# Performance work log

Hardware: AMD Instinct MI355X
Metric: run time of the kernel (lower is better)

The kernel has to match this reference:

```python
import jax, jax.numpy as jnp
import numpy as np

DECAY_FACTOR = 0.995  # temporal decay applied to similarities
MIN_SIMILARITY = 0.0

BATCH, FEAT_DIM = 256, 128
CAPACITY, HORIZON, NUM_FEATURES = 100000, 24, 7


def _l2_normalize(x, eps=1e-12):
    # matches torch F.normalize(p=2): divide by max(||x||, eps)
    n = jnp.linalg.norm(x, axis=-1, keepdims=True)
    return x / jnp.maximum(n, eps)


def setup_inputs() -> dict:
    key = jax.random.key(0)
    k1, k2, k3, k4 = jax.random.split(key, 4)
    return {
        "query": jax.random.normal(k1, (BATCH, FEAT_DIM), dtype=jnp.float32),
        "keys": jax.random.normal(k2, (CAPACITY, FEAT_DIM), dtype=jnp.float32),
        "values": jax.random.normal(k3, (CAPACITY, HORIZON, NUM_FEATURES), dtype=jnp.float32),
        "timestamps": jax.random.randint(k4, (CAPACITY,), 0, 1000, dtype=jnp.int32),
        "global_step": 1000,
        "top_k": 5,
    }


def reference(query, keys, values, timestamps, global_step, top_k):
    """ErrorMemoryBank.retrieve with a full bank (n == capacity),
    no trajectory bias, min_similarity=0."""
    q_norm = _l2_normalize(query)            # [B, D]
    k_norm = _l2_normalize(keys)             # [C, D]
    sims = jnp.einsum('bd,cd->bc', q_norm, k_norm)  # [B, C] cosine sims

    age = (jnp.asarray(global_step, jnp.int32) - timestamps).astype(jnp.float32)  # [C]
    decay = jnp.power(jnp.float32(DECAY_FACTOR), age)                              # [C]
    sims = sims * decay[None, :]

    top_sims, top_idx = jax.lax.top_k(sims, top_k)   # [B, K], [B, K]
    retrieved = values[top_idx]                      # gather -> [B, K, H, F]
    valid_mask = top_sims >= MIN_SIMILARITY          # [B, K]
    return retrieved, top_sims, valid_mask, top_idx
```

## Files before the change

### kernel.cpp

```cpp
#include <hip/hip_runtime.h>
#include <math.h>

#define BATCH 256
#define FEAT 128
#define CAP 100000
#define ROWF 168
#define K 5
#define NBLKG 1564
#define NCHK 6256
#define NCHKR 6250
#define SCPT 7
#define MAXSEL 48
#define MARGIN 0.008f

#define OUT_SIMS 215040
#define OUT_MASK 216320
#define OUT_IDX  217600

#define WS_QF    0
#define WS_TMAX  16384

typedef __attribute__((ext_vector_type(8))) short short8;
typedef __attribute__((ext_vector_type(4))) float f32x4;

#define BET(vs,vi,ss,ii) ((vs) > (ss) || ((vs) == (ss) && (vi) < (ii)))

__device__ __forceinline__ unsigned pack2(float a, float b) {
  unsigned ua = (__float_as_uint(a) + 0x8000u) >> 16;
  unsigned ub = (__float_as_uint(b) + 0x8000u) & 0xffff0000u;
  return ua | ub;
}

__device__ __forceinline__ void ins_val(float v, float (&s)[5]) {
  if (v > s[4]) {
    float x = v;
    #pragma unroll
    for (int j = 0; j < 5; ++j) {
      float hi = fmaxf(s[j], x);
      x = fminf(s[j], x);
      s[j] = hi;
    }
  }
}

__device__ __forceinline__ void ins_cmp(float v, int k, float (&s)[5], int (&i)[5]) {
  if (BET(v,k,s[4],i[4])) {
    if (BET(v,k,s[3],i[3])) { s[4]=s[3]; i[4]=i[3];
      if (BET(v,k,s[2],i[2])) { s[3]=s[2]; i[3]=i[2];
        if (BET(v,k,s[1],i[1])) { s[2]=s[1]; i[2]=i[1];
          if (BET(v,k,s[0],i[0])) { s[1]=s[0]; i[1]=i[0]; s[0]=v; i[0]=k; }
          else { s[1]=v; i[1]=k; } }
        else { s[2]=v; i[2]=k; } }
      else { s[3]=v; i[3]=k; } }
    else { s[4]=v; i[4]=k; }
  }
}

__global__ __launch_bounds__(256) void prep_q(const float* __restrict__ query,
                                              uint4* __restrict__ qF) {
  int b = blockIdx.x, tid = threadIdx.x;
  int rid = tid >> 4, dp = tid & 15;
  int q_ = b*16 + rid;
  const float4* src = reinterpret_cast<const float4*>(query + (size_t)q_*FEAT + dp*8);
  float4 v0 = src[0], v1 = src[1];
  float ss = v0.x*v0.x + v0.y*v0.y + v0.z*v0.z + v0.w*v0.w
           + v1.x*v1.x + v1.y*v1.y + v1.z*v1.z + v1.w*v1.w;
  ss += __shfl_xor(ss,1); ss += __shfl_xor(ss,2);
  ss += __shfl_xor(ss,4); ss += __shfl_xor(ss,8);
  float inv = 1.0f / fmaxf(sqrtf(ss), 1e-12f);
  v0.x*=inv; v0.y*=inv; v0.z*=inv; v0.w*=inv;
  v1.x*=inv; v1.y*=inv; v1.z*=inv; v1.w*=inv;
  uint4 pk;
  pk.x = pack2(v0.x,v0.y); pk.y = pack2(v0.z,v0.w);
  pk.z = pack2(v1.x,v1.y); pk.w = pack2(v1.z,v1.w);
  int s_ = dp >> 2, lg = dp & 3;
  qF[(b*4 + s_)*64 + lg*16 + rid] = pk;
}

__global__ __launch_bounds__(512, 4) void gemm_max6(
    const float* __restrict__ keys, const int* __restrict__ ts,
    const int* __restrict__ gstep, const uint4* __restrict__ qF,
    float* __restrict__ tmax) {
  __shared__ uint4 lds_kf[16*66];
  __shared__ float sscale[64];
  int tid = threadIdx.x;
  int w = tid >> 6, lane = tid & 63;
  int blk = blockIdx.x;
  int kbase = blk * 64;
  int g0 = gstep[0];

  short8 qf0[4], qf1[4];
  #pragma unroll
  for (int s_ = 0; s_ < 4; ++s_) {
    qf0[s_] = __builtin_bit_cast(short8, qF[((2*w  )*4 + s_)*64 + lane]);
    qf1[s_] = __builtin_bit_cast(short8, qF[((2*w+1)*4 + s_)*64 + lane]);
  }

  int dp = tid & 15;
  #pragma unroll
  for (int it = 0; it < 2; ++it) {
    int kl = it*32 + (tid >> 4);
    int gk = kbase + kl;
    int gkc = gk < CAP ? gk : CAP-1;
    const float4* kp = reinterpret_cast<const float4*>(keys + (size_t)gkc*FEAT + dp*8);
    float4 v0 = kp[0], v1 = kp[1];
    float ss = v0.x*v0.x+v0.y*v0.y+v0.z*v0.z+v0.w*v0.w
             + v1.x*v1.x+v1.y*v1.y+v1.z*v1.z+v1.w*v1.w;
    ss += __shfl_xor(ss,1); ss += __shfl_xor(ss,2);
    ss += __shfl_xor(ss,4); ss += __shfl_xor(ss,8);
    if (dp == 0) {
      float scl = 0.0f;
      if (gk < CAP) {
        float age = (float)(g0 - ts[gk]);
        scl = exp2f(age * -0.00723157f) * __frsqrt_rn(fmaxf(ss, 1e-24f));
      }
      sscale[kl] = scl;
    }
    uint4 pk;
    pk.x = pack2(v0.x, v0.y); pk.y = pack2(v0.z, v0.w);
    pk.z = pack2(v1.x, v1.y); pk.w = pack2(v1.z, v1.w);
    int slab = (kl >> 4)*4 + (dp >> 2);
    int slot = (dp & 3)*16 + (kl & 15);
    lds_kf[slab*66 + slot] = pk;
  }
  __syncthreads();

  float tm0[4], tm1[4];
  #pragma unroll
  for (int t = 0; t < 4; ++t) {
    f32x4 acc0 = {0.f,0.f,0.f,0.f}, acc1 = {0.f,0.f,0.f,0.f};
    #pragma unroll
    for (int s_ = 0; s_ < 4; ++s_) {
      short8 a = __builtin_bit_cast(short8, lds_kf[(t*4 + s_)*66 + lane]);
      acc0 = __builtin_amdgcn_mfma_f32_16x16x32_bf16(a, qf0[s_], acc0, 0,0,0);
      acc1 = __builtin_amdgcn_mfma_f32_16x16x32_bf16(a, qf1[s_], acc1, 0,0,0);
    }
    int kbl = t*16 + (lane>>4)*4;
    float4 sc = *reinterpret_cast<float4*>(&sscale[kbl]);
    float m0 = fmaxf(fmaxf(acc0[0]*sc.x, acc0[1]*sc.y),
                     fmaxf(acc0[2]*sc.z, acc0[3]*sc.w));
    float m1 = fmaxf(fmaxf(acc1[0]*sc.x, acc1[1]*sc.y),
                     fmaxf(acc1[2]*sc.z, acc1[3]*sc.w));
    m0 = fmaxf(m0, __shfl_xor(m0,16)); m0 = fmaxf(m0, __shfl_xor(m0,32));
    m1 = fmaxf(m1, __shfl_xor(m1,16)); m1 = fmaxf(m1, __shfl_xor(m1,32));
    tm0[t] = m0; tm1[t] = m1;
  }

  if (lane < 16) {
    int q0 = w*32 + lane, q1 = q0 + 16;
    float4 a0 = {tm0[0],tm0[1],tm0[2],tm0[3]};
    float4 b0 = {tm1[0],tm1[1],tm1[2],tm1[3]};
    *reinterpret_cast<float4*>(&tmax[(size_t)q0*NCHK + blk*4]) = a0;
    *reinterpret_cast<float4*>(&tmax[(size_t)q1*NCHK + blk*4]) = b0;
  }
}

__global__ __launch_bounds__(1024) void select_rescore4(
    const float* __restrict__ tmax, const float* __restrict__ keys,
    const float* __restrict__ query, const int* __restrict__ ts,
    const int* __restrict__ gstep, const float* __restrict__ values,
    float* __restrict__ out) {
  int q = blockIdx.x, tid = threadIdx.x;
  int w = tid >> 6, lane = tid & 63;
  int gstep0 = gstep[0];

  __shared__ float qrow[FEAT];
  if (tid < 16) {
    int d0 = tid * 8;
    const float4* src = reinterpret_cast<const float4*>(query + (size_t)q*FEAT + d0);
    float4 v0 = src[0], v1 = src[1];
    float ss = v0.x*v0.x + v0.y*v0.y + v0.z*v0.z + v0.w*v0.w
             + v1.x*v1.x + v1.y*v1.y + v1.z*v1.z + v1.w*v1.w;
    ss += __shfl_xor(ss,1); ss += __shfl_xor(ss,2);
    ss += __shfl_xor(ss,4); ss += __shfl_xor(ss,8);
    float inv = 1.0f / fmaxf(sqrtf(ss), 1e-12f);
    v0.x*=inv; v0.y*=inv; v0.z*=inv; v0.w*=inv;
    v1.x*=inv; v1.y*=inv; v1.z*=inv; v1.w*=inv;
    float4* dst = reinterpret_cast<float4*>(qrow + d0);
    dst[0] = v0; dst[1] = v1;
  }
  __syncthreads();

  float cs[SCPT];
  #pragma unroll
  for (int j = 0; j < SCPT; ++j) {
    int c = tid + j*1024;
    cs[j] = (c < NCHKR) ? tmax[(size_t)q*NCHK + c] : -INFINITY;
  }
  float s5[5] = {-INFINITY,-INFINITY,-INFINITY,-INFINITY,-INFINITY};
  #pragma unroll
  for (int j = 0; j < SCPT; ++j) ins_val(cs[j], s5);
  #pragma unroll
  for (int off = 1; off < 64; off <<= 1) {
    float ps[5];
    #pragma unroll
    for (int j=0;j<5;++j) ps[j] = __shfl_xor(s5[j], off);
    #pragma unroll
    for (int j=0;j<5;++j) ins_val(ps[j], s5);
  }
  __shared__ float rS[16][5]; __shared__ int rI[16][5];
  if (lane == 0) {
    #pragma unroll
    for (int j=0;j<5;++j) rS[w][j] = s5[j];
  }
  __syncthreads();
  __shared__ float thSh;
  if (w == 0) {
    float m5[5] = {-INFINITY,-INFINITY,-INFINITY,-INFINITY,-INFINITY};
    if (lane < 16) {
      #pragma unroll
      for (int j=0;j<5;++j) m5[j] = rS[lane][j];
    }
    #pragma unroll
    for (int off = 1; off < 16; off <<= 1) {
      float ps[5];
      #pragma unroll
      for (int j=0;j<5;++j) ps[j] = __shfl_xor(m5[j], off);
      #pragma unroll
      for (int j=0;j<5;++j) ins_val(ps[j], m5);
    }
    if (lane == 0) thSh = m5[4] - MARGIN;
  }
  __syncthreads();
  float th = thSh;

  __shared__ int cnt; __shared__ int clist[MAXSEL];
  if (tid == 0) cnt = 0;
  __syncthreads();
  #pragma unroll
  for (int j = 0; j < SCPT; ++j) {
    int c = tid + j*1024;
    if (c < NCHKR && cs[j] >= th) {
      int p = atomicAdd(&cnt, 1);
      if (p < MAXSEL) clist[p] = c;
    }
  }
  __syncthreads();
  int nsel = cnt < MAXSEL ? cnt : MAXSEL;

  __shared__ float exs[MAXSEL*16];
  for (int s4 = tid; s4 < nsel*64; s4 += 1024) {
    int slot = s4 >> 2, part = s4 & 3;
    int key = clist[slot >> 4]*16 + (slot & 15);
    float dot = 0.f, ksq = 0.f;
    if (key < CAP) {
      const float4* kp = reinterpret_cast<const float4*>(keys + (size_t)key*FEAT + part*32);
      const float4* qp = reinterpret_cast<float4*>(qrow) + part*8;
      #pragma unroll
      for (int d = 0; d < 8; ++d) {
        float4 kv = kp[d];
        float4 qv = qp[d];
        dot = fmaf(kv.w,qv.w,fmaf(kv.z,qv.z,fmaf(kv.y,qv.y,fmaf(kv.x,qv.x,dot))));
        ksq = fmaf(kv.w,kv.w,fmaf(kv.z,kv.z,fmaf(kv.y,kv.y,fmaf(kv.x,kv.x,ksq))));
      }
    }
    dot += __shfl_xor(dot,1); dot += __shfl_xor(dot,2);
    ksq += __shfl_xor(ksq,1); ksq += __shfl_xor(ksq,2);
    if (part == 0) {
      float sim = -INFINITY;
      if (key < CAP) {
        float age = (float)(gstep0 - ts[key]);
        sim = dot / fmaxf(sqrtf(ksq), 1e-12f) * powf(0.995f, age);
      }
      exs[slot] = sim;
    }
  }
  __syncthreads();

  float fs5[5] = {-INFINITY,-INFINITY,-INFINITY,-INFINITY,-INFINITY};
  int   fi5[5] = {0x7fffffff,0x7fffffff,0x7fffffff,0x7fffffff,0x7fffffff};
  if (tid < nsel*16) {
    fs5[0] = exs[tid];
    fi5[0] = clist[tid >> 4]*16 + (tid & 15);
  }
  #pragma unroll
  for (int off = 1; off < 64; off <<= 1) {
    float ps[5]; int pi[5];
    #pragma unroll
    for (int j=0;j<5;++j){ ps[j]=__shfl_xor(fs5[j],off); pi[j]=__shfl_xor(fi5[j],off); }
    #pragma unroll
    for (int j=0;j<5;++j) ins_cmp(ps[j], pi[j], fs5, fi5);
  }
  if (lane == 0) {
    #pragma unroll
    for (int j=0;j<5;++j){ rS[w][j]=fs5[j]; rI[w][j]=fi5[j]; }
  }
  __syncthreads();
  __shared__ int wix[K];
  if (w == 0) {
    float fs[5] = {-INFINITY,-INFINITY,-INFINITY,-INFINITY,-INFINITY};
    int   fi[5] = {0x7fffffff,0x7fffffff,0x7fffffff,0x7fffffff,0x7fffffff};
    if (lane < 16) {
      #pragma unroll
      for (int j=0;j<5;++j){ fs[j]=rS[lane][j]; fi[j]=rI[lane][j]; }
    }
    #pragma unroll
    for (int off = 1; off < 16; off <<= 1) {
      float ps[5]; int pi[5];
      #pragma unroll
      for (int j=0;j<5;++j){ ps[j]=__shfl_xor(fs[j],off); pi[j]=__shfl_xor(fi[j],off); }
      #pragma unroll
      for (int j=0;j<5;++j) ins_cmp(ps[j], pi[j], fs, fi);
    }
    if (lane == 0) {
      #pragma unroll
      for (int r = 0; r < K; ++r) {
        out[OUT_SIMS + q*K + r] = fs[r];
        out[OUT_MASK + q*K + r] = (fs[r] >= 0.0f) ? 1.0f : 0.0f;
        out[OUT_IDX  + q*K + r] = (float)fi[r];
        wix[r] = fi[r];
      }
    }
  }
  __syncthreads();
  for (int idx = tid; idx < K*ROWF; idx += 1024) {
    int r = idx / ROWF, e = idx - r*ROWF;
    out[(q*K + r)*ROWF + e] = values[(size_t)wix[r]*ROWF + e];
  }
}

extern "C" void kernel_launch(void* const* d_in, const int* in_sizes, int n_in,
                              void* d_out, int out_size, void* d_ws, size_t ws_size,
                              hipStream_t stream) {
  const float* query  = (const float*)d_in[0];
  const float* keys   = (const float*)d_in[1];
  const float* values = (const float*)d_in[2];
  const int*   ts     = (const int*)d_in[3];
  const int*   gstep  = (const int*)d_in[4];

  float* out  = (float*)d_out;
  float* wsf  = (float*)d_ws;
  uint4* qF   = (uint4*)(wsf + WS_QF);
  float* tmax = wsf + WS_TMAX;

  prep_q<<<16, 256, 0, stream>>>(query, qF);
  gemm_max6<<<NBLKG, 512, 0, stream>>>(keys, ts, gstep, qF, tmax);
  select_rescore4<<<BATCH, 1024, 0, stream>>>(tmax, keys, query, ts, gstep, values, out);
}
```

Before: 46.54 us.

## Fuse three kernels into one persistent kernel with a grid barrier

```diff
diff --git a/kernel.cpp b/kernel.cpp
--- a/kernel.cpp
+++ b/kernel.cpp
@@ -6,7 +6,8 @@
 #define CAP 100000
 #define ROWF 168
 #define K 5
-#define NBLKG 1564
+#define NBLOCKS 256
+#define NCHKB 1564
 #define NCHK 6256
 #define NCHKR 6250
 #define SCPT 7
@@ -17,8 +18,8 @@
 #define OUT_MASK 216320
 #define OUT_IDX  217600
 
-#define WS_QF    0
-#define WS_TMAX  16384
+#define WS_TMAX 0
+#define WS_BAR  1601536
 
 typedef __attribute__((ext_vector_type(8))) short short8;
 typedef __attribute__((ext_vector_type(4))) float f32x4;
@@ -56,115 +57,125 @@
   }
 }
 
-__global__ __launch_bounds__(256) void prep_q(const float* __restrict__ query,
-                                              uint4* __restrict__ qF) {
-  int b = blockIdx.x, tid = threadIdx.x;
-  int rid = tid >> 4, dp = tid & 15;
-  int q_ = b*16 + rid;
-  const float4* src = reinterpret_cast<const float4*>(query + (size_t)q_*FEAT + dp*8);
-  float4 v0 = src[0], v1 = src[1];
-  float ss = v0.x*v0.x + v0.y*v0.y + v0.z*v0.z + v0.w*v0.w
-           + v1.x*v1.x + v1.y*v1.y + v1.z*v1.z + v1.w*v1.w;
-  ss += __shfl_xor(ss,1); ss += __shfl_xor(ss,2);
-  ss += __shfl_xor(ss,4); ss += __shfl_xor(ss,8);
-  float inv = 1.0f / fmaxf(sqrtf(ss), 1e-12f);
-  v0.x*=inv; v0.y*=inv; v0.z*=inv; v0.w*=inv;
-  v1.x*=inv; v1.y*=inv; v1.z*=inv; v1.w*=inv;
-  uint4 pk;
-  pk.x = pack2(v0.x,v0.y); pk.y = pack2(v0.z,v0.w);
-  pk.z = pack2(v1.x,v1.y); pk.w = pack2(v1.z,v1.w);
-  int s_ = dp >> 2, lg = dp & 3;
-  qF[(b*4 + s_)*64 + lg*16 + rid] = pk;
-}
-
-__global__ __launch_bounds__(512, 4) void gemm_max6(
-    const float* __restrict__ keys, const int* __restrict__ ts,
-    const int* __restrict__ gstep, const uint4* __restrict__ qF,
-    float* __restrict__ tmax) {
-  __shared__ uint4 lds_kf[16*66];
-  __shared__ float sscale[64];
+__global__ __launch_bounds__(1024, 4) void fused_all(
+    const float* __restrict__ query, const float* __restrict__ keys,
+    const float* __restrict__ values, const int* __restrict__ ts,
+    const int* __restrict__ gstep, float* __restrict__ tmax,
+    unsigned* __restrict__ bar, float* __restrict__ out) {
+  __shared__ uint4 shmem[4096];
+  __shared__ __attribute__((aligned(16))) float sscale[2][64];
+  __shared__ float qrow[FEAT];
+  __shared__ float rS[16][5]; __shared__ int rI[16][5];
+  __shared__ float thSh;
+  __shared__ int cnt_s; __shared__ int clist[MAXSEL];
+  __shared__ float exs[MAXSEL*16];
+  __shared__ int wix[K];
+
   int tid = threadIdx.x;
   int w = tid >> 6, lane = tid & 63;
   int blk = blockIdx.x;
-  int kbase = blk * 64;
   int g0 = gstep[0];
 
-  short8 qf0[4], qf1[4];
-  #pragma unroll
-  for (int s_ = 0; s_ < 4; ++s_) {
-    qf0[s_] = __builtin_bit_cast(short8, qF[((2*w  )*4 + s_)*64 + lane]);
-    qf1[s_] = __builtin_bit_cast(short8, qF[((2*w+1)*4 + s_)*64 + lane]);
-  }
-
+  {
+    int dp = lane & 15;
+    #pragma unroll
+    for (int it = 0; it < 4; ++it) {
+      int rid = it*4 + (lane >> 4);
+      int q_ = w*16 + rid;
+      const float4* src = reinterpret_cast<const float4*>(query + (size_t)q_*FEAT + dp*8);
+      float4 v0 = src[0], v1 = src[1];
+      float ss = v0.x*v0.x + v0.y*v0.y + v0.z*v0.z + v0.w*v0.w
+               + v1.x*v1.x + v1.y*v1.y + v1.z*v1.z + v1.w*v1.w;
+      ss += __shfl_xor(ss,1); ss += __shfl_xor(ss,2);
+      ss += __shfl_xor(ss,4); ss += __shfl_xor(ss,8);
+      float inv = 1.0f / fmaxf(sqrtf(ss), 1e-12f);
+      v0.x*=inv; v0.y*=inv; v0.z*=inv; v0.w*=inv;
+      v1.x*=inv; v1.y*=inv; v1.z*=inv; v1.w*=inv;
+      uint4 pk;
+      pk.x = pack2(v0.x,v0.y); pk.y = pack2(v0.z,v0.w);
+      pk.z = pack2(v1.x,v1.y); pk.w = pack2(v1.z,v1.w);
+      shmem[w*256 + (dp>>2)*64 + (dp&3)*16 + rid] = pk;
+    }
+  }
+  __syncthreads();
+  short8 qf[4];
+  #pragma unroll
+  for (int s_ = 0; s_ < 4; ++s_)
+    qf[s_] = __builtin_bit_cast(short8, shmem[w*256 + s_*64 + lane]);
+  __syncthreads();
+
+  int kl = tid >> 4;
   int dp = tid & 15;
-  #pragma unroll
-  for (int it = 0; it < 2; ++it) {
-    int kl = it*32 + (tid >> 4);
-    int gk = kbase + kl;
+  float4 kv0, kv1; int tsv = 0;
+  auto ld = [&](int cb) {
+    int gk = cb*64 + kl;
     int gkc = gk < CAP ? gk : CAP-1;
     const float4* kp = reinterpret_cast<const float4*>(keys + (size_t)gkc*FEAT + dp*8);
-    float4 v0 = kp[0], v1 = kp[1];
-    float ss = v0.x*v0.x+v0.y*v0.y+v0.z*v0.z+v0.w*v0.w
-             + v1.x*v1.x+v1.y*v1.y+v1.z*v1.z+v1.w*v1.w;
+    kv0 = kp[0]; kv1 = kp[1];
+    if (dp == 0 && gk < CAP) tsv = ts[gk];
+  };
+  int buf = 0;
+  int cb = blk;
+  ld(cb);
+  while (cb < NCHKB) {
+    float ss = kv0.x*kv0.x+kv0.y*kv0.y+kv0.z*kv0.z+kv0.w*kv0.w
+             + kv1.x*kv1.x+kv1.y*kv1.y+kv1.z*kv1.z+kv1.w*kv1.w;
     ss += __shfl_xor(ss,1); ss += __shfl_xor(ss,2);
     ss += __shfl_xor(ss,4); ss += __shfl_xor(ss,8);
     if (dp == 0) {
       float scl = 0.0f;
+      int gk = cb*64 + kl;
       if (gk < CAP) {
-        float age = (float)(g0 - ts[gk]);
+        float age = (float)(g0 - tsv);
         scl = exp2f(age * -0.00723157f) * __frsqrt_rn(fmaxf(ss, 1e-24f));
       }
-      sscale[kl] = scl;
+      sscale[buf][kl] = scl;
     }
     uint4 pk;
-    pk.x = pack2(v0.x, v0.y); pk.y = pack2(v0.z, v0.w);
-    pk.z = pack2(v1.x, v1.y); pk.w = pack2(v1.z, v1.w);
+    pk.x = pack2(kv0.x, kv0.y); pk.y = pack2(kv0.z, kv0.w);
+    pk.z = pack2(kv1.x, kv1.y); pk.w = pack2(kv1.z, kv1.w);
     int slab = (kl >> 4)*4 + (dp >> 2);
     int slot = (dp & 3)*16 + (kl & 15);
-    lds_kf[slab*66 + slot] = pk;
-  }
-  __syncthreads();
-
-  float tm0[4], tm1[4];
-  #pragma unroll
-  for (int t = 0; t < 4; ++t) {
-    f32x4 acc0 = {0.f,0.f,0.f,0.f}, acc1 = {0.f,0.f,0.f,0.f};
-    #pragma unroll
-    for (int s_ = 0; s_ < 4; ++s_) {
-      short8 a = __builtin_bit_cast(short8, lds_kf[(t*4 + s_)*66 + lane]);
-      acc0 = __builtin_amdgcn_mfma_f32_16x16x32_bf16(a, qf0[s_], acc0, 0,0,0);
-      acc1 = __builtin_amdgcn_mfma_f32_16x16x32_bf16(a, qf1[s_], acc1, 0,0,0);
-    }
-    int kbl = t*16 + (lane>>4)*4;
-    float4 sc = *reinterpret_cast<float4*>(&sscale[kbl]);
-    float m0 = fmaxf(fmaxf(acc0[0]*sc.x, acc0[1]*sc.y),
-                     fmaxf(acc0[2]*sc.z, acc0[3]*sc.w));
-    float m1 = fmaxf(fmaxf(acc1[0]*sc.x, acc1[1]*sc.y),
-                     fmaxf(acc1[2]*sc.z, acc1[3]*sc.w));
-    m0 = fmaxf(m0, __shfl_xor(m0,16)); m0 = fmaxf(m0, __shfl_xor(m0,32));
-    m1 = fmaxf(m1, __shfl_xor(m1,16)); m1 = fmaxf(m1, __shfl_xor(m1,32));
-    tm0[t] = m0; tm1[t] = m1;
-  }
-
-  if (lane < 16) {
-    int q0 = w*32 + lane, q1 = q0 + 16;
-    float4 a0 = {tm0[0],tm0[1],tm0[2],tm0[3]};
-    float4 b0 = {tm1[0],tm1[1],tm1[2],tm1[3]};
-    *reinterpret_cast<float4*>(&tmax[(size_t)q0*NCHK + blk*4]) = a0;
-    *reinterpret_cast<float4*>(&tmax[(size_t)q1*NCHK + blk*4]) = b0;
-  }
-}
-
-__global__ __launch_bounds__(1024) void select_rescore4(
-    const float* __restrict__ tmax, const float* __restrict__ keys,
-    const float* __restrict__ query, const int* __restrict__ ts,
-    const int* __restrict__ gstep, const float* __restrict__ values,
-    float* __restrict__ out) {
-  int q = blockIdx.x, tid = threadIdx.x;
-  int w = tid >> 6, lane = tid & 63;
-  int gstep0 = gstep[0];
-
-  __shared__ float qrow[FEAT];
+    shmem[buf*1056 + slab*66 + slot] = pk;
+    __syncthreads();
+
+    int nb = cb + NBLOCKS;
+    if (nb < NCHKB) ld(nb);
+
+    float tm[4];
+    #pragma unroll
+    for (int t = 0; t < 4; ++t) {
+      f32x4 acc = {0.f,0.f,0.f,0.f};
+      #pragma unroll
+      for (int s_ = 0; s_ < 4; ++s_) {
+        short8 a = __builtin_bit_cast(short8, shmem[buf*1056 + (t*4 + s_)*66 + lane]);
+        acc = __builtin_amdgcn_mfma_f32_16x16x32_bf16(a, qf[s_], acc, 0,0,0);
+      }
+      int kbl = t*16 + (lane>>4)*4;
+      float4 sc = *reinterpret_cast<float4*>(&sscale[buf][kbl]);
+      float m = fmaxf(fmaxf(acc[0]*sc.x, acc[1]*sc.y),
+                      fmaxf(acc[2]*sc.z, acc[3]*sc.w));
+      m = fmaxf(m, __shfl_xor(m,16));
+      m = fmaxf(m, __shfl_xor(m,32));
+      tm[t] = m;
+    }
+    if (lane < 16) {
+      float4 a0 = {tm[0],tm[1],tm[2],tm[3]};
+      *reinterpret_cast<float4*>(&tmax[(size_t)(w*16+lane)*NCHK + cb*4]) = a0;
+    }
+    buf ^= 1; cb = nb;
+  }
+
+  __syncthreads();
+  if (tid == 0) {
+    __threadfence();
+    __hip_atomic_fetch_add(bar, 1u, __ATOMIC_ACQ_REL, __HIP_MEMORY_SCOPE_AGENT);
+    while (__hip_atomic_load(bar, __ATOMIC_ACQUIRE, __HIP_MEMORY_SCOPE_AGENT) < NBLOCKS) {}
+  }
+  __syncthreads();
+  __threadfence();
+
+  int q = blk;
   if (tid < 16) {
     int d0 = tid * 8;
     const float4* src = reinterpret_cast<const float4*>(query + (size_t)q*FEAT + d0);
@@ -198,13 +209,11 @@
     #pragma unroll
     for (int j=0;j<5;++j) ins_val(ps[j], s5);
   }
-  __shared__ float rS[16][5]; __shared__ int rI[16][5];
   if (lane == 0) {
     #pragma unroll
     for (int j=0;j<5;++j) rS[w][j] = s5[j];
   }
   __syncthreads();
-  __shared__ float thSh;
   if (w == 0) {
     float m5[5] = {-INFINITY,-INFINITY,-INFINITY,-INFINITY,-INFINITY};
     if (lane < 16) {
@@ -224,21 +233,19 @@
   __syncthreads();
   float th = thSh;
 
-  __shared__ int cnt; __shared__ int clist[MAXSEL];
-  if (tid == 0) cnt = 0;
+  if (tid == 0) cnt_s = 0;
   __syncthreads();
   #pragma unroll
   for (int j = 0; j < SCPT; ++j) {
     int c = tid + j*1024;
     if (c < NCHKR && cs[j] >= th) {
-      int p = atomicAdd(&cnt, 1);
+      int p = atomicAdd(&cnt_s, 1);
       if (p < MAXSEL) clist[p] = c;
     }
   }
   __syncthreads();
-  int nsel = cnt < MAXSEL ? cnt : MAXSEL;
-
-  __shared__ float exs[MAXSEL*16];
+  int nsel = cnt_s < MAXSEL ? cnt_s : MAXSEL;
+
   for (int s4 = tid; s4 < nsel*64; s4 += 1024) {
     int slot = s4 >> 2, part = s4 & 3;
     int key = clist[slot >> 4]*16 + (slot & 15);
@@ -259,7 +266,7 @@
     if (part == 0) {
       float sim = -INFINITY;
       if (key < CAP) {
-        float age = (float)(gstep0 - ts[key]);
+        float age = (float)(g0 - ts[key]);
         sim = dot / fmaxf(sqrtf(ksq), 1e-12f) * powf(0.995f, age);
       }
       exs[slot] = sim;
@@ -286,7 +293,6 @@
     for (int j=0;j<5;++j){ rS[w][j]=fs5[j]; rI[w][j]=fi5[j]; }
   }
   __syncthreads();
-  __shared__ int wix[K];
   if (w == 0) {
     float fs[5] = {-INFINITY,-INFINITY,-INFINITY,-INFINITY,-INFINITY};
     int   fi[5] = {0x7fffffff,0x7fffffff,0x7fffffff,0x7fffffff,0x7fffffff};
@@ -330,10 +336,10 @@
 
   float* out  = (float*)d_out;
   float* wsf  = (float*)d_ws;
-  uint4* qF   = (uint4*)(wsf + WS_QF);
   float* tmax = wsf + WS_TMAX;
-
-  prep_q<<<16, 256, 0, stream>>>(query, qF);
-  gemm_max6<<<NBLKG, 512, 0, stream>>>(keys, ts, gstep, qF, tmax);
-  select_rescore4<<<BATCH, 1024, 0, stream>>>(tmax, keys, query, ts, gstep, values, out);
-}
+  unsigned* bar = (unsigned*)(wsf + WS_BAR);
+
+  hipMemsetAsync(bar, 0, sizeof(unsigned), stream);
+  fused_all<<<NBLOCKS, 1024, 0, stream>>>(query, keys, values, ts, gstep,
+                                          tmax, bar, out);
+}
```

New measurement: 140.2 us. 3.01x slower.
